# Kernel optimization log

Hardware: AMD Instinct MI355X
Metric: run time of the kernel (lower is better)

Reference implementation:

```python
import jax, jax.numpy as jnp
import numpy as np

B, D_IN, D_OUT, E, TOP_K = 8192, 1024, 512, 8, 2  # D_OUT here is gate hidden = D_IN//2
OUT_DIM = 1024
LN_EPS = 1e-5


def setup_inputs() -> dict:
    key = jax.random.key(0)
    ks = jax.random.split(key, 5)
    s_in = 1.0 / np.sqrt(D_IN)
    s_h = 1.0 / np.sqrt(D_OUT)
    return {
        "x": jax.random.normal(ks[0], (B, D_IN), jnp.float32),
        "gate_w1": jax.random.normal(ks[1], (D_IN, D_OUT), jnp.float32) * s_in,
        "gate_b1": jnp.zeros((D_OUT,), jnp.float32),
        "gate_w2": jax.random.normal(ks[2], (D_OUT, E), jnp.float32) * s_h,
        "gate_b2": jnp.zeros((E,), jnp.float32),
        "We": jax.random.normal(ks[3], (E, D_IN, OUT_DIM), jnp.float32) * s_in,
        "be": jnp.zeros((E, OUT_DIM), jnp.float32),
        "ln_g": jnp.ones((E, OUT_DIM), jnp.float32),
        "ln_b": jnp.zeros((E, OUT_DIM), jnp.float32),
    }


def reference(x, gate_w1, gate_b1, gate_w2, gate_b2, We, be, ln_g, ln_b):
    # Gating network: Linear -> GELU (exact) -> Linear
    g = jax.nn.gelu(x @ gate_w1 + gate_b1, approximate=False)
    scores = g @ gate_w2 + gate_b2                       # [B, E]
    topk_s, topk_i = jax.lax.top_k(scores, TOP_K)        # [B, K]
    topk_w = jax.nn.softmax(topk_s, axis=-1)             # softmax over the top-k only
    # Scatter top-k weights into dense per-expert weights [B, E]
    rows = jnp.arange(scores.shape[0])[:, None]
    dense_w = jnp.zeros_like(scores).at[rows, topk_i].add(topk_w)
    # All-expert forward (non-selected experts get weight 0): Linear -> LayerNorm -> GELU
    h = jnp.einsum("bi,eio->beo", x, We) + be            # [B, E, O]
    mu = h.mean(axis=-1, keepdims=True)
    var = jnp.mean(jnp.square(h - mu), axis=-1, keepdims=True)
    h = (h - mu) * jax.lax.rsqrt(var + LN_EPS) * ln_g + ln_b
    h = jax.nn.gelu(h, approximate=False)
    # Weighted combine (Dropout is identity in eval mode)
    return jnp.einsum("beo,be->bo", h, dense_w)          # [B, O]
```

## Files before the change

### kernel.cpp

```cpp
#include <hip/hip_runtime.h>
#include <hip/hip_bf16.h>
#include <math.h>

#define B_ROWS 8192
#define D_INK  1024
#define D_H    512
#define N_E    8
#define OUT_D  1024
#define LN_EPS 1e-5f
#define GAP_TAU 3e-3f

typedef _Float16 f16x8 __attribute__((ext_vector_type(8)));
typedef _Float16 f16x4v __attribute__((ext_vector_type(4)));
typedef float    f32x4  __attribute__((ext_vector_type(4)));

#define GLOBAL_AS __attribute__((address_space(1)))
#define LDS_AS    __attribute__((address_space(3)))

__device__ __forceinline__ void async16(const void* gptr, void* lptr) {
  __builtin_amdgcn_global_load_lds((const GLOBAL_AS unsigned int*)gptr,
                                   (LDS_AS unsigned int*)lptr, 16, 0, 0);
}

__device__ __forceinline__ float gelu_exact(float x) {
  return 0.5f * x * (1.0f + erff(x * 0.707106781186547524f));
}
__device__ __forceinline__ float clamp_diag(float v) {
  return fminf(fmaxf(v, -1e15f), 1e15f);
}

__global__ __launch_bounds__(256) void convert_x_kernel(
    const float4* __restrict__ x4, f16x4v* __restrict__ hi4) {
  int i = blockIdx.x * 256 + threadIdx.x;
  float4 v = x4[i];
  f16x4v h;
  h[0] = (_Float16)v.x; h[1] = (_Float16)v.y;
  h[2] = (_Float16)v.z; h[3] = (_Float16)v.w;
  hi4[i] = h;
}

__global__ void transpose_split_kernel(const float* __restrict__ src,
                                       _Float16* __restrict__ hi,
                                       int R, int C) {
  __shared__ float tile[32][33];
  long base = (long)blockIdx.z * R * C;
  int c0 = blockIdx.x * 32, r0 = blockIdx.y * 32;
  int tx = threadIdx.x, ty = threadIdx.y;
#pragma unroll
  for (int i = ty; i < 32; i += 8)
    tile[i][tx] = src[base + (long)(r0 + i) * C + (c0 + tx)];
  __syncthreads();
#pragma unroll
  for (int i = ty; i < 32; i += 8)
    hi[base + (long)(c0 + i) * R + (r0 + tx)] = (_Float16)tile[tx][i];
}


__global__ __launch_bounds__(256) void gate_gemm_kernel(
    const _Float16* __restrict__ xh, const _Float16* __restrict__ wh,
    const float* __restrict__ b1, float* __restrict__ g) {
  __shared__ __align__(16) unsigned short Ah[128 * 64];
  __shared__ __align__(16) unsigned short Bh[128 * 64];
  int tid = threadIdx.x, lane = tid & 63, wave = tid >> 6;
  int wm = wave >> 1, wn = wave & 1;
  int n0 = blockIdx.x * 128, m0 = blockIdx.y * 128;

  const char* pah[4]; const char* pbh[4];
#pragma unroll
  for (int i = 0; i < 4; ++i) {
    int f = i * 256 + tid;
    int rowt = f >> 3, slot = f & 7;
    int seg = slot ^ (rowt & 7);
    pah[i] = (const char*)xh + (long)(m0 + rowt) * (D_INK * 2) + seg * 16;
    pbh[i] = (const char*)wh + (long)(n0 + rowt) * (D_INK * 2) + seg * 16;
  }
  f32x4 acc[4][4];
#pragma unroll
  for (int mi = 0; mi < 4; ++mi)
#pragma unroll
    for (int ni = 0; ni < 4; ++ni) acc[mi][ni] = (f32x4){0.f, 0.f, 0.f, 0.f};

  int cl = lane & 15, quad = lane >> 4;
  for (int k0 = 0; k0 < D_INK; k0 += 64) {
#pragma unroll
    for (int i = 0; i < 4; ++i) {
      async16(pah[i] + (long)k0 * 2, (char*)Ah + (i * 256 + wave * 64) * 16);
      async16(pbh[i] + (long)k0 * 2, (char*)Bh + (i * 256 + wave * 64) * 16);
    }
    __syncthreads();
#pragma unroll
    for (int ks = 0; ks < 2; ++ks) {
      f16x8 ah[4], bh[4];
#pragma unroll
      for (int mi = 0; mi < 4; ++mi) {
        int row = wm * 64 + mi * 16 + cl;
        ah[mi] = *(const f16x8*)((const char*)Ah + row * 128 +
                                 (((ks * 4 + quad) ^ (cl & 7)) * 16));
      }
#pragma unroll
      for (int ni = 0; ni < 4; ++ni) {
        int row = wn * 64 + ni * 16 + cl;
        bh[ni] = *(const f16x8*)((const char*)Bh + row * 128 +
                                 (((ks * 4 + quad) ^ (cl & 7)) * 16));
      }
#pragma unroll
      for (int mi = 0; mi < 4; ++mi)
#pragma unroll
        for (int ni = 0; ni < 4; ++ni)
          acc[mi][ni] = __builtin_amdgcn_mfma_f32_16x16x32_f16(ah[mi], bh[ni], acc[mi][ni], 0, 0, 0);
    }
    __syncthreads();
  }
#pragma unroll
  for (int mi = 0; mi < 4; ++mi)
#pragma unroll
    for (int r = 0; r < 4; ++r) {
      int row = m0 + wm * 64 + mi * 16 + quad * 4 + r;
#pragma unroll
      for (int ni = 0; ni < 4; ++ni) {
        int col = n0 + wn * 64 + ni * 16 + cl;
        float v = clamp_diag(acc[mi][ni][r] + b1[col]);
        g[(long)row * D_H + col] = gelu_exact(v);
      }
    }
}

__global__ __launch_bounds__(256) void score_kernel(
    const float* __restrict__ g, const float* __restrict__ w2,
    const float* __restrict__ b2, float* __restrict__ scores,
    int* __restrict__ nflag, int* __restrict__ worklist) {
  int tid = threadIdx.x, lane = tid & 63, wave = tid >> 6;
  int b = blockIdx.x * 4 + wave;
  const float* grow = g + (long)b * D_H + lane * 8;
  float4 g0 = *(const float4*)grow;
  float4 g1 = *(const float4*)(grow + 4);
  float gv[8] = {g0.x, g0.y, g0.z, g0.w, g1.x, g1.y, g1.z, g1.w};
  float acc[8];
#pragma unroll
  for (int e = 0; e < 8; ++e) acc[e] = 0.f;
#pragma unroll
  for (int j = 0; j < 8; ++j) {
    const float* wrow = w2 + (lane * 8 + j) * N_E;
#pragma unroll
    for (int e = 0; e < 8; ++e) acc[e] += gv[j] * wrow[e];
  }
#pragma unroll
  for (int off = 32; off >= 1; off >>= 1)
#pragma unroll
    for (int e = 0; e < 8; ++e) acc[e] += __shfl_xor(acc[e], off, 64);
  if (lane == 0) {
    float s[8];
#pragma unroll
    for (int e = 0; e < 8; ++e) { s[e] = acc[e] + b2[e]; scores[b * N_E + e] = s[e]; }
    int i0 = 0;
#pragma unroll
    for (int e = 1; e < 8; ++e) if (s[e] > s[i0]) i0 = e;
    int i1 = (i0 == 0) ? 1 : 0;
#pragma unroll
    for (int e = 0; e < 8; ++e) if (e != i0 && s[e] > s[i1]) i1 = e;
    float s2 = -3e38f;
#pragma unroll
    for (int e = 0; e < 8; ++e) if (e != i0 && e != i1 && s[e] > s2) s2 = s[e];
    if (s[i1] - s2 < GAP_TAU) {
      int idx = atomicAdd(nflag, 1);
      worklist[idx] = b;
    }
  }
}

__global__ __launch_bounds__(256) void fixup_g_kernel(
    const float* __restrict__ x, const float* __restrict__ w1,
    const float* __restrict__ b1, const int* __restrict__ nflag,
    const int* __restrict__ worklist, double* __restrict__ g64) {
  int n = *nflag;
  int total = n * 2;
  for (int t = blockIdx.x; t < total; t += gridDim.x) {
    int w = t >> 1, half = t & 1;
    int row = worklist[w];
    int col = half * 256 + threadIdx.x;
    const float* xr = x + (long)row * D_INK;
    double a0 = 0.0, a1 = 0.0, a2 = 0.0, a3 = 0.0;
    for (int k = 0; k < D_INK; k += 4) {
      a0 += (double)xr[k + 0] * (double)w1[(long)(k + 0) * D_H + col];
      a1 += (double)xr[k + 1] * (double)w1[(long)(k + 1) * D_H + col];
      a2 += (double)xr[k + 2] * (double)w1[(long)(k + 2) * D_H + col];
      a3 += (double)xr[k + 3] * (double)w1[(long)(k + 3) * D_H + col];
    }
    double s = ((a0 + a1) + (a2 + a3)) + (double)b1[col];
    g64[(long)w * D_H + col] = 0.5 * s * (1.0 + erf(s * 0.70710678118654752440));
  }
}

__global__ __launch_bounds__(256) void fixup_score_kernel(
    const double* __restrict__ g64, const float* __restrict__ w2,
    const float* __restrict__ b2, const int* __restrict__ nflag,
    const int* __restrict__ worklist, float* __restrict__ scores) {
  __shared__ double p2[256];
  int n = *nflag;
  int tid = threadIdx.x;
  for (int w = blockIdx.x; w < n; w += gridDim.x) {
    int row = worklist[w];
    int e = tid & 7, seg = tid >> 3;
    double s = 0.0;
#pragma unroll
    for (int q = seg * 16; q < seg * 16 + 16; ++q)
      s += g64[(long)w * D_H + q] * (double)w2[q * N_E + e];
    p2[tid] = s;
    __syncthreads();
    if (tid < N_E) {
      double t = 0.0;
      for (int i = 0; i < 32; ++i) t += p2[i * 8 + tid];
      scores[row * N_E + tid] = (float)(t + (double)b2[tid]);
    }
    __syncthreads();
  }
}

__global__ __launch_bounds__(256) void select_kernel(
    const float* __restrict__ scores, int* __restrict__ counts,
    int* __restrict__ bucket, float* __restrict__ pair_w,
    int* __restrict__ pair_e) {
  __shared__ int lcnt[N_E];
  __shared__ int lbase[N_E];
  int tid = threadIdx.x;
  int b = blockIdx.x * 256 + tid;
  if (tid < N_E) lcnt[tid] = 0;
  __syncthreads();
  float s[8];
#pragma unroll
  for (int e = 0; e < 8; ++e) s[e] = scores[b * N_E + e];
  int i0 = 0;
#pragma unroll
  for (int e = 1; e < 8; ++e) if (s[e] > s[i0]) i0 = e;
  int i1 = (i0 == 0) ? 1 : 0;
#pragma unroll
  for (int e = 0; e < 8; ++e) if (e != i0 && s[e] > s[i1]) i1 = e;
  float z = expf(s[i1] - s[i0]);
  float inv = 1.0f / (1.0f + z);
  int r0 = atomicAdd(&lcnt[i0], 1);
  int r1 = atomicAdd(&lcnt[i1], 1);
  __syncthreads();
  if (tid < N_E) lbase[tid] = atomicAdd(&counts[tid], lcnt[tid]);
  __syncthreads();
  int p0 = 2 * b, p1 = 2 * b + 1;
  pair_e[p0] = i0; pair_w[p0] = inv;
  pair_e[p1] = i1; pair_w[p1] = z * inv;
  bucket[i0 * B_ROWS + lbase[i0] + r0] = p0;
  bucket[i1 * B_ROWS + lbase[i1] + r1] = p1;
}

__global__ __launch_bounds__(512) void expert_gemm_kernel(
    const _Float16* __restrict__ xh, const _Float16* __restrict__ wet,
    const int* __restrict__ counts, const int* __restrict__ bucket,
    __bf16* __restrict__ h) {
  int nt = blockIdx.x, mt = blockIdx.y, e = blockIdx.z;
  int cnt = counts[e];
  if (mt * 256 >= cnt) return;
  __shared__ __align__(16) unsigned short As[256 * 64];
  __shared__ __align__(16) unsigned short Bs[256 * 64];
  __shared__ int dest_s[256];
  int tid = threadIdx.x, lane = tid & 63, wave = tid >> 6;
  int wm = wave >> 2, wn = wave & 3;
  int n0 = nt * 256;
  if (tid < 256) {
    int idx = mt * 256 + tid;
    dest_s[tid] = (idx < cnt) ? bucket[e * B_ROWS + idx] : 0;
  }
  __syncthreads();
  const char* xb = (const char*)xh;
  const char* wb = (const char*)wet + (long)e * (D_INK * OUT_D * 2);
  const char* aptr[4];
  const char* bptr[4];
#pragma unroll
  for (int i = 0; i < 4; ++i) {
    int f = i * 512 + tid;
    int rowt = f >> 3, slot = f & 7;
    int seg = slot ^ (rowt & 7);
    int rowid = dest_s[rowt] >> 1;
    aptr[i] = xb + (long)rowid * (D_INK * 2) + seg * 16;
    bptr[i] = wb + (long)(n0 + rowt) * (D_INK * 2) + seg * 16;
  }
  f32x4 acc[8][4];
#pragma unroll
  for (int mi = 0; mi < 8; ++mi)
#pragma unroll
    for (int ni = 0; ni < 4; ++ni) acc[mi][ni] = (f32x4){0.f, 0.f, 0.f, 0.f};

  int cl = lane & 15, quad = lane >> 4;
  for (int k0 = 0; k0 < D_INK; k0 += 64) {
#pragma unroll
    for (int i = 0; i < 4; ++i) {
      async16(aptr[i] + (long)k0 * 2, (char*)As + (i * 512 + wave * 64) * 16);
      async16(bptr[i] + (long)k0 * 2, (char*)Bs + (i * 512 + wave * 64) * 16);
    }
    __syncthreads();
#pragma unroll
    for (int ks = 0; ks < 2; ++ks) {
      f16x8 bfr[4];
#pragma unroll
      for (int ni = 0; ni < 4; ++ni) {
        int row = wn * 64 + ni * 16 + cl;
        bfr[ni] = *(const f16x8*)((const char*)Bs + row * 128 +
                                  (((ks * 4 + quad) ^ (cl & 7)) * 16));
      }
#pragma unroll
      for (int mi = 0; mi < 8; ++mi) {
        int row = wm * 128 + mi * 16 + cl;
        f16x8 af = *(const f16x8*)((const char*)As + row * 128 +
                                   (((ks * 4 + quad) ^ (cl & 7)) * 16));
#pragma unroll
        for (int ni = 0; ni < 4; ++ni)
          acc[mi][ni] = __builtin_amdgcn_mfma_f32_16x16x32_f16(af, bfr[ni], acc[mi][ni], 0, 0, 0);
      }
    }
    __syncthreads();
  }
#pragma unroll
  for (int mi = 0; mi < 8; ++mi)
#pragma unroll
    for (int r = 0; r < 4; ++r) {
      int row256 = wm * 128 + mi * 16 + quad * 4 + r;
      if (mt * 256 + row256 < cnt) {
        long dest = dest_s[row256];
        __bf16* hp = h + dest * OUT_D + n0 + wn * 64 + cl;
#pragma unroll
        for (int ni = 0; ni < 4; ++ni)
          hp[ni * 16] = (__bf16)clamp_diag(acc[mi][ni][r]);
      }
    }
}

__global__ __launch_bounds__(256) void ln_combine_kernel(
    const __bf16* __restrict__ h, const float* __restrict__ pair_w,
    const int* __restrict__ pair_e, const float* __restrict__ be,
    const float* __restrict__ ln_g, const float* __restrict__ ln_b,
    float* __restrict__ out) {
  int b = blockIdx.x, tid = threadIdx.x;
  int lane = tid & 63, wave = tid >> 6;
  int c0 = tid * 4;
  __shared__ float red[4][4];
  float hv[2][4];
  float stats[4];
  int ei[2]; float wi[2];
#pragma unroll
  for (int k = 0; k < 2; ++k) {
    int p = 2 * b + k;
    ei[k] = pair_e[p]; wi[k] = pair_w[p];
    const unsigned short* hp = (const unsigned short*)(h + (long)p * OUT_D) + c0;
    ushort4 raw = *(const ushort4*)hp;
    float4 bev = *(const float4*)(be + ei[k] * OUT_D + c0);
    float v0 = __uint_as_float((unsigned)raw.x << 16) + bev.x;
    float v1 = __uint_as_float((unsigned)raw.y << 16) + bev.y;
    float v2 = __uint_as_float((unsigned)raw.z << 16) + bev.z;
    float v3 = __uint_as_float((unsigned)raw.w << 16) + bev.w;
    hv[k][0] = v0; hv[k][1] = v1; hv[k][2] = v2; hv[k][3] = v3;
    stats[2 * k] = v0 + v1 + v2 + v3;
    stats[2 * k + 1] = v0 * v0 + v1 * v1 + v2 * v2 + v3 * v3;
  }
#pragma unroll
  for (int off = 32; off >= 1; off >>= 1)
#pragma unroll
    for (int i = 0; i < 4; ++i) stats[i] += __shfl_xor(stats[i], off, 64);
  if (lane == 0) {
#pragma unroll
    for (int i = 0; i < 4; ++i) red[wave][i] = stats[i];
  }
  __syncthreads();
  float tot[4] = {0.f, 0.f, 0.f, 0.f};
#pragma unroll
  for (int w = 0; w < 4; ++w)
#pragma unroll
    for (int i = 0; i < 4; ++i) tot[i] += red[w][i];
  float outv[4] = {0.f, 0.f, 0.f, 0.f};
#pragma unroll
  for (int k = 0; k < 2; ++k) {
    float mean = tot[2 * k] * (1.0f / OUT_D);
    float var = tot[2 * k + 1] * (1.0f / OUT_D) - mean * mean;
    float rstd = rsqrtf(fmaxf(var, 0.f) + LN_EPS);
    float4 gp = *(const float4*)(ln_g + ei[k] * OUT_D + c0);
    float4 bp = *(const float4*)(ln_b + ei[k] * OUT_D + c0);
    float t0 = (hv[k][0] - mean) * rstd * gp.x + bp.x;
    float t1 = (hv[k][1] - mean) * rstd * gp.y + bp.y;
    float t2 = (hv[k][2] - mean) * rstd * gp.z + bp.z;
    float t3 = (hv[k][3] - mean) * rstd * gp.w + bp.w;
    outv[0] += wi[k] * gelu_exact(t0);
    outv[1] += wi[k] * gelu_exact(t1);
    outv[2] += wi[k] * gelu_exact(t2);
    outv[3] += wi[k] * gelu_exact(t3);
  }
  float4 o; o.x = outv[0]; o.y = outv[1]; o.z = outv[2]; o.w = outv[3];
  *(float4*)(out + (long)b * OUT_D + c0) = o;
}

extern "C" void kernel_launch(void* const* d_in, const int* in_sizes, int n_in,
                              void* d_out, int out_size, void* d_ws, size_t ws_size,
                              hipStream_t stream) {
  const float* x       = (const float*)d_in[0];
  const float* gate_w1 = (const float*)d_in[1];
  const float* gate_b1 = (const float*)d_in[2];
  const float* gate_w2 = (const float*)d_in[3];
  const float* gate_b2 = (const float*)d_in[4];
  const float* We      = (const float*)d_in[5];
  const float* be      = (const float*)d_in[6];
  const float* ln_g    = (const float*)d_in[7];
  const float* ln_b    = (const float*)d_in[8];
  float* out = (float*)d_out;

  char* ws = (char*)d_ws;
  size_t off = 0;
  _Float16* x16h = (_Float16*)(ws + off); off += (size_t)B_ROWS * D_INK * 2;
  _Float16* w1th = (_Float16*)(ws + off); off += (size_t)D_H * D_INK * 2;
  _Float16* wet  = (_Float16*)(ws + off); off += (size_t)N_E * D_INK * OUT_D * 2;
  float* g       = (float*)(ws + off); off += (size_t)B_ROWS * D_H * 4;
  float* scores  = (float*)(ws + off); off += (size_t)B_ROWS * N_E * 4;
  int* counts    = (int*)(ws + off);   off += 64;
  int* nflag     = counts + 8;
  int* worklist  = (int*)(ws + off);   off += (size_t)B_ROWS * 4;
  int* bucket    = (int*)(ws + off);   off += (size_t)N_E * B_ROWS * 4;
  float* pair_w  = (float*)(ws + off); off += (size_t)2 * B_ROWS * 4;
  int* pair_e    = (int*)(ws + off);   off += (size_t)2 * B_ROWS * 4;
  __bf16* h      = (__bf16*)(ws + off); off += (size_t)2 * B_ROWS * OUT_D * 2;
  double* g64    = (double*)h;

  hipMemsetAsync(counts, 0, 64, stream);
  convert_x_kernel<<<B_ROWS * D_INK / 4 / 256, 256, 0, stream>>>(
      (const float4*)x, (f16x4v*)x16h);
  transpose_split_kernel<<<dim3(D_H / 32, D_INK / 32, 1), dim3(32, 8), 0, stream>>>(
      gate_w1, w1th, D_INK, D_H);
  transpose_split_kernel<<<dim3(OUT_D / 32, D_INK / 32, N_E), dim3(32, 8), 0, stream>>>(
      We, wet, D_INK, OUT_D);
  gate_gemm_kernel<<<dim3(D_H / 128, B_ROWS / 128), 256, 0, stream>>>(
      x16h, w1th, gate_b1, g);
  score_kernel<<<B_ROWS / 4, 256, 0, stream>>>(
      g, gate_w2, gate_b2, scores, nflag, worklist);
  fixup_g_kernel<<<512, 256, 0, stream>>>(
      x, gate_w1, gate_b1, nflag, worklist, g64);
  fixup_score_kernel<<<128, 256, 0, stream>>>(
      g64, gate_w2, gate_b2, nflag, worklist, scores);
  select_kernel<<<B_ROWS / 256, 256, 0, stream>>>(
      scores, counts, bucket, pair_w, pair_e);
  expert_gemm_kernel<<<dim3(OUT_D / 256, B_ROWS / 256, N_E), 512, 0, stream>>>(
      x16h, wet, counts, bucket, h);
  ln_combine_kernel<<<B_ROWS, 256, 0, stream>>>(
      h, pair_w, pair_e, be, ln_g, ln_b, out);
}
```

Baseline: 322.8 us.

## Double-buffer LDS in gate and expert GEMMs, shrink expert tiles to 128

Result: no change. 324.8 us (+0.6%).

```diff
diff --git a/kernel.cpp b/kernel.cpp
--- a/kernel.cpp
+++ b/kernel.cpp
@@ -56,11 +56,47 @@
 }
 
 
+__device__ __forceinline__ void stage8(const char* const (&ap)[4],
+                                       const char* const (&bp)[4], long koff,
+                                       char* Ab, char* Bb, int wave) {
+#pragma unroll
+  for (int i = 0; i < 4; ++i) {
+    async16(ap[i] + koff, Ab + (i * 256 + wave * 64) * 16);
+    async16(bp[i] + koff, Bb + (i * 256 + wave * 64) * 16);
+  }
+}
+
+__device__ __forceinline__ void tile_compute(const char* Ab, const char* Bb,
+                                             int wm, int wn, int cl, int quad,
+                                             f32x4 (&acc)[4][4]) {
+#pragma unroll
+  for (int ks = 0; ks < 2; ++ks) {
+    f16x8 ah[4], bh[4];
+#pragma unroll
+    for (int mi = 0; mi < 4; ++mi) {
+      int row = wm * 64 + mi * 16 + cl;
+      ah[mi] = *(const f16x8*)(Ab + row * 128 + (((ks * 4 + quad) ^ (cl & 7)) * 16));
+    }
+#pragma unroll
+    for (int ni = 0; ni < 4; ++ni) {
+      int row = wn * 64 + ni * 16 + cl;
+      bh[ni] = *(const f16x8*)(Bb + row * 128 + (((ks * 4 + quad) ^ (cl & 7)) * 16));
+    }
+#pragma unroll
+    for (int mi = 0; mi < 4; ++mi)
+#pragma unroll
+      for (int ni = 0; ni < 4; ++ni)
+        acc[mi][ni] = __builtin_amdgcn_mfma_f32_16x16x32_f16(ah[mi], bh[ni], acc[mi][ni], 0, 0, 0);
+  }
+}
+
 __global__ __launch_bounds__(256) void gate_gemm_kernel(
     const _Float16* __restrict__ xh, const _Float16* __restrict__ wh,
     const float* __restrict__ b1, float* __restrict__ g) {
-  __shared__ __align__(16) unsigned short Ah[128 * 64];
-  __shared__ __align__(16) unsigned short Bh[128 * 64];
+  __shared__ __align__(16) unsigned short Ah0[128 * 64];
+  __shared__ __align__(16) unsigned short Bh0[128 * 64];
+  __shared__ __align__(16) unsigned short Ah1[128 * 64];
+  __shared__ __align__(16) unsigned short Bh1[128 * 64];
   int tid = threadIdx.x, lane = tid & 63, wave = tid >> 6;
   int wm = wave >> 1, wn = wave & 1;
   int n0 = blockIdx.x * 128, m0 = blockIdx.y * 128;
@@ -81,34 +117,14 @@
     for (int ni = 0; ni < 4; ++ni) acc[mi][ni] = (f32x4){0.f, 0.f, 0.f, 0.f};
 
   int cl = lane & 15, quad = lane >> 4;
-  for (int k0 = 0; k0 < D_INK; k0 += 64) {
-#pragma unroll
-    for (int i = 0; i < 4; ++i) {
-      async16(pah[i] + (long)k0 * 2, (char*)Ah + (i * 256 + wave * 64) * 16);
-      async16(pbh[i] + (long)k0 * 2, (char*)Bh + (i * 256 + wave * 64) * 16);
-    }
-    __syncthreads();
-#pragma unroll
-    for (int ks = 0; ks < 2; ++ks) {
-      f16x8 ah[4], bh[4];
-#pragma unroll
-      for (int mi = 0; mi < 4; ++mi) {
-        int row = wm * 64 + mi * 16 + cl;
-        ah[mi] = *(const f16x8*)((const char*)Ah + row * 128 +
-                                 (((ks * 4 + quad) ^ (cl & 7)) * 16));
-      }
-#pragma unroll
-      for (int ni = 0; ni < 4; ++ni) {
-        int row = wn * 64 + ni * 16 + cl;
-        bh[ni] = *(const f16x8*)((const char*)Bh + row * 128 +
-                                 (((ks * 4 + quad) ^ (cl & 7)) * 16));
-      }
-#pragma unroll
-      for (int mi = 0; mi < 4; ++mi)
-#pragma unroll
-        for (int ni = 0; ni < 4; ++ni)
-          acc[mi][ni] = __builtin_amdgcn_mfma_f32_16x16x32_f16(ah[mi], bh[ni], acc[mi][ni], 0, 0, 0);
-    }
+  stage8(pah, pbh, 0, (char*)Ah0, (char*)Bh0, wave);
+  __syncthreads();
+  for (int s = 0; s < 16; s += 2) {
+    stage8(pah, pbh, (long)(s + 1) * 128, (char*)Ah1, (char*)Bh1, wave);
+    tile_compute((const char*)Ah0, (const char*)Bh0, wm, wn, cl, quad, acc);
+    __syncthreads();
+    if (s + 2 < 16) stage8(pah, pbh, (long)(s + 2) * 128, (char*)Ah0, (char*)Bh0, wave);
+    tile_compute((const char*)Ah1, (const char*)Bh1, wm, wn, cl, quad, acc);
     __syncthreads();
   }
 #pragma unroll
@@ -249,21 +265,25 @@
   bucket[i1 * B_ROWS + lbase[i1] + r1] = p1;
 }
 
-__global__ __launch_bounds__(512) void expert_gemm_kernel(
+__global__ __launch_bounds__(256) void expert_gemm_kernel(
     const _Float16* __restrict__ xh, const _Float16* __restrict__ wet,
     const int* __restrict__ counts, const int* __restrict__ bucket,
     __bf16* __restrict__ h) {
-  int nt = blockIdx.x, mt = blockIdx.y, e = blockIdx.z;
+  int bid = blockIdx.x;
+  int e = bid & 7, seq = bid >> 3;
+  int mt = seq >> 3, nt = seq & 7;
   int cnt = counts[e];
-  if (mt * 256 >= cnt) return;
-  __shared__ __align__(16) unsigned short As[256 * 64];
-  __shared__ __align__(16) unsigned short Bs[256 * 64];
-  __shared__ int dest_s[256];
+  if (mt * 128 >= cnt) return;
+  __shared__ __align__(16) unsigned short As0[128 * 64];
+  __shared__ __align__(16) unsigned short Bs0[128 * 64];
+  __shared__ __align__(16) unsigned short As1[128 * 64];
+  __shared__ __align__(16) unsigned short Bs1[128 * 64];
+  __shared__ int dest_s[128];
   int tid = threadIdx.x, lane = tid & 63, wave = tid >> 6;
-  int wm = wave >> 2, wn = wave & 3;
-  int n0 = nt * 256;
-  if (tid < 256) {
-    int idx = mt * 256 + tid;
+  int wm = wave >> 1, wn = wave & 1;
+  int n0 = nt * 128;
+  if (tid < 128) {
+    int idx = mt * 128 + tid;
     dest_s[tid] = (idx < cnt) ? bucket[e * B_ROWS + idx] : 0;
   }
   __syncthreads();
@@ -273,55 +293,37 @@
   const char* bptr[4];
 #pragma unroll
   for (int i = 0; i < 4; ++i) {
-    int f = i * 512 + tid;
+    int f = i * 256 + tid;
     int rowt = f >> 3, slot = f & 7;
     int seg = slot ^ (rowt & 7);
     int rowid = dest_s[rowt] >> 1;
     aptr[i] = xb + (long)rowid * (D_INK * 2) + seg * 16;
     bptr[i] = wb + (long)(n0 + rowt) * (D_INK * 2) + seg * 16;
   }
-  f32x4 acc[8][4];
-#pragma unroll
-  for (int mi = 0; mi < 8; ++mi)
+  f32x4 acc[4][4];
+#pragma unroll
+  for (int mi = 0; mi < 4; ++mi)
 #pragma unroll
     for (int ni = 0; ni < 4; ++ni) acc[mi][ni] = (f32x4){0.f, 0.f, 0.f, 0.f};
 
   int cl = lane & 15, quad = lane >> 4;
-  for (int k0 = 0; k0 < D_INK; k0 += 64) {
-#pragma unroll
-    for (int i = 0; i < 4; ++i) {
-      async16(aptr[i] + (long)k0 * 2, (char*)As + (i * 512 + wave * 64) * 16);
-      async16(bptr[i] + (long)k0 * 2, (char*)Bs + (i * 512 + wave * 64) * 16);
-    }
-    __syncthreads();
-#pragma unroll
-    for (int ks = 0; ks < 2; ++ks) {
-      f16x8 bfr[4];
-#pragma unroll
-      for (int ni = 0; ni < 4; ++ni) {
-        int row = wn * 64 + ni * 16 + cl;
-        bfr[ni] = *(const f16x8*)((const char*)Bs + row * 128 +
-                                  (((ks * 4 + quad) ^ (cl & 7)) * 16));
-      }
-#pragma unroll
-      for (int mi = 0; mi < 8; ++mi) {
-        int row = wm * 128 + mi * 16 + cl;
-        f16x8 af = *(const f16x8*)((const char*)As + row * 128 +
-                                   (((ks * 4 + quad) ^ (cl & 7)) * 16));
-#pragma unroll
-        for (int ni = 0; ni < 4; ++ni)
-          acc[mi][ni] = __builtin_amdgcn_mfma_f32_16x16x32_f16(af, bfr[ni], acc[mi][ni], 0, 0, 0);
-      }
-    }
-    __syncthreads();
-  }
-#pragma unroll
-  for (int mi = 0; mi < 8; ++mi)
+  stage8(aptr, bptr, 0, (char*)As0, (char*)Bs0, wave);
+  __syncthreads();
+  for (int s = 0; s < 16; s += 2) {
+    stage8(aptr, bptr, (long)(s + 1) * 128, (char*)As1, (char*)Bs1, wave);
+    tile_compute((const char*)As0, (const char*)Bs0, wm, wn, cl, quad, acc);
+    __syncthreads();
+    if (s + 2 < 16) stage8(aptr, bptr, (long)(s + 2) * 128, (char*)As0, (char*)Bs0, wave);
+    tile_compute((const char*)As1, (const char*)Bs1, wm, wn, cl, quad, acc);
+    __syncthreads();
+  }
+#pragma unroll
+  for (int mi = 0; mi < 4; ++mi)
 #pragma unroll
     for (int r = 0; r < 4; ++r) {
-      int row256 = wm * 128 + mi * 16 + quad * 4 + r;
-      if (mt * 256 + row256 < cnt) {
-        long dest = dest_s[row256];
+      int row128 = wm * 64 + mi * 16 + quad * 4 + r;
+      if (mt * 128 + row128 < cnt) {
+        long dest = dest_s[row128];
         __bf16* hp = h + dest * OUT_D + n0 + wn * 64 + cl;
 #pragma unroll
         for (int ni = 0; ni < 4; ++ni)
@@ -439,7 +441,7 @@
       g64, gate_w2, gate_b2, nflag, worklist, scores);
   select_kernel<<<B_ROWS / 256, 256, 0, stream>>>(
       scores, counts, bucket, pair_w, pair_e);
-  expert_gemm_kernel<<<dim3(OUT_D / 256, B_ROWS / 256, N_E), 512, 0, stream>>>(
+  expert_gemm_kernel<<<N_E * (B_ROWS / 128) * (OUT_D / 128), 256, 0, stream>>>(
       x16h, wet, counts, bucket, h);
   ln_combine_kernel<<<B_ROWS, 256, 0, stream>>>(
       h, pair_w, pair_e, be, ln_g, ln_b, out);
```

## Double-buffer expert GEMM LDS tiles and interleave prefetch with MFMA phases

Applied to the files above, without the earlier changes.

Result: slower. 334.2 us (+3.5%).

```diff
diff --git a/kernel.cpp b/kernel.cpp
--- a/kernel.cpp
+++ b/kernel.cpp
@@ -56,6 +56,40 @@
 }
 
 
+__device__ __forceinline__ void stage8(const char* const (&ap)[4],
+                                       const char* const (&bp)[4], long koff,
+                                       char* Ab, char* Bb, int wave) {
+#pragma unroll
+  for (int i = 0; i < 4; ++i) {
+    async16(ap[i] + koff, Ab + (i * 256 + wave * 64) * 16);
+    async16(bp[i] + koff, Bb + (i * 256 + wave * 64) * 16);
+  }
+}
+
+__device__ __forceinline__ void tile_compute(const char* Ab, const char* Bb,
+                                             int wm, int wn, int cl, int quad,
+                                             f32x4 (&acc)[4][4]) {
+#pragma unroll
+  for (int ks = 0; ks < 2; ++ks) {
+    f16x8 ah[4], bh[4];
+#pragma unroll
+    for (int mi = 0; mi < 4; ++mi) {
+      int row = wm * 64 + mi * 16 + cl;
+      ah[mi] = *(const f16x8*)(Ab + row * 128 + (((ks * 4 + quad) ^ (cl & 7)) * 16));
+    }
+#pragma unroll
+    for (int ni = 0; ni < 4; ++ni) {
+      int row = wn * 64 + ni * 16 + cl;
+      bh[ni] = *(const f16x8*)(Bb + row * 128 + (((ks * 4 + quad) ^ (cl & 7)) * 16));
+    }
+#pragma unroll
+    for (int mi = 0; mi < 4; ++mi)
+#pragma unroll
+      for (int ni = 0; ni < 4; ++ni)
+        acc[mi][ni] = __builtin_amdgcn_mfma_f32_16x16x32_f16(ah[mi], bh[ni], acc[mi][ni], 0, 0, 0);
+  }
+}
+
 __global__ __launch_bounds__(256) void gate_gemm_kernel(
     const _Float16* __restrict__ xh, const _Float16* __restrict__ wh,
     const float* __restrict__ b1, float* __restrict__ g) {
@@ -82,33 +116,9 @@
 
   int cl = lane & 15, quad = lane >> 4;
   for (int k0 = 0; k0 < D_INK; k0 += 64) {
-#pragma unroll
-    for (int i = 0; i < 4; ++i) {
-      async16(pah[i] + (long)k0 * 2, (char*)Ah + (i * 256 + wave * 64) * 16);
-      async16(pbh[i] + (long)k0 * 2, (char*)Bh + (i * 256 + wave * 64) * 16);
-    }
+    stage8(pah, pbh, (long)k0 * 2, (char*)Ah, (char*)Bh, wave);
     __syncthreads();
-#pragma unroll
-    for (int ks = 0; ks < 2; ++ks) {
-      f16x8 ah[4], bh[4];
-#pragma unroll
-      for (int mi = 0; mi < 4; ++mi) {
-        int row = wm * 64 + mi * 16 + cl;
-        ah[mi] = *(const f16x8*)((const char*)Ah + row * 128 +
-                                 (((ks * 4 + quad) ^ (cl & 7)) * 16));
-      }
-#pragma unroll
-      for (int ni = 0; ni < 4; ++ni) {
-        int row = wn * 64 + ni * 16 + cl;
-        bh[ni] = *(const f16x8*)((const char*)Bh + row * 128 +
-                                 (((ks * 4 + quad) ^ (cl & 7)) * 16));
-      }
-#pragma unroll
-      for (int mi = 0; mi < 4; ++mi)
-#pragma unroll
-        for (int ni = 0; ni < 4; ++ni)
-          acc[mi][ni] = __builtin_amdgcn_mfma_f32_16x16x32_f16(ah[mi], bh[ni], acc[mi][ni], 0, 0, 0);
-    }
+    tile_compute((const char*)Ah, (const char*)Bh, wm, wn, cl, quad, acc);
     __syncthreads();
   }
 #pragma unroll
@@ -256,8 +266,8 @@
   int nt = blockIdx.x, mt = blockIdx.y, e = blockIdx.z;
   int cnt = counts[e];
   if (mt * 256 >= cnt) return;
-  __shared__ __align__(16) unsigned short As[256 * 64];
-  __shared__ __align__(16) unsigned short Bs[256 * 64];
+  __shared__ __align__(16) unsigned short As[2][256 * 64];
+  __shared__ __align__(16) unsigned short Bs[2][256 * 64];
   __shared__ int dest_s[256];
   int tid = threadIdx.x, lane = tid & 63, wave = tid >> 6;
   int wm = wave >> 2, wn = wave & 3;
@@ -267,17 +277,14 @@
     dest_s[tid] = (idx < cnt) ? bucket[e * B_ROWS + idx] : 0;
   }
   __syncthreads();
-  const char* xb = (const char*)xh;
   const char* wb = (const char*)wet + (long)e * (D_INK * OUT_D * 2);
-  const char* aptr[4];
-  const char* bptr[4];
+  const char* aptr[4]; const char* bptr[4];
 #pragma unroll
   for (int i = 0; i < 4; ++i) {
     int f = i * 512 + tid;
     int rowt = f >> 3, slot = f & 7;
     int seg = slot ^ (rowt & 7);
-    int rowid = dest_s[rowt] >> 1;
-    aptr[i] = xb + (long)rowid * (D_INK * 2) + seg * 16;
+    aptr[i] = (const char*)xh + (long)(dest_s[rowt] >> 1) * (D_INK * 2) + seg * 16;
     bptr[i] = wb + (long)(n0 + rowt) * (D_INK * 2) + seg * 16;
   }
   f32x4 acc[8][4];
@@ -287,33 +294,58 @@
     for (int ni = 0; ni < 4; ++ni) acc[mi][ni] = (f32x4){0.f, 0.f, 0.f, 0.f};
 
   int cl = lane & 15, quad = lane >> 4;
-  for (int k0 = 0; k0 < D_INK; k0 += 64) {
-#pragma unroll
-    for (int i = 0; i < 4; ++i) {
-      async16(aptr[i] + (long)k0 * 2, (char*)As + (i * 512 + wave * 64) * 16);
-      async16(bptr[i] + (long)k0 * 2, (char*)Bs + (i * 512 + wave * 64) * 16);
-    }
-    __syncthreads();
-#pragma unroll
-    for (int ks = 0; ks < 2; ++ks) {
-      f16x8 bfr[4];
+#pragma unroll
+  for (int i = 0; i < 4; ++i) {
+    async16(aptr[i], (char*)As[0] + (i * 512 + wave * 64) * 16);
+    async16(bptr[i], (char*)Bs[0] + (i * 512 + wave * 64) * 16);
+  }
+  asm volatile("s_waitcnt vmcnt(0)" ::: "memory");
+  __builtin_amdgcn_s_barrier();
+
+  for (int t = 0; t < 16; ++t) {
+    int cur = t & 1;
+    const char* Ab = (const char*)As[cur];
+    const char* Bb = (const char*)Bs[cur];
+    char* An = (char*)As[cur ^ 1];
+    char* Bn = (char*)Bs[cur ^ 1];
+    long koff = (long)(t + 1) * 128;
+#pragma unroll
+    for (int q = 0; q < 4; ++q) {
+      if (t < 15) {
+        if (q == 0) {
+#pragma unroll
+          for (int i = 0; i < 4; ++i)
+            async16(aptr[i] + koff, An + (i * 512 + wave * 64) * 16);
+        } else if (q == 1) {
+#pragma unroll
+          for (int i = 0; i < 4; ++i)
+            async16(bptr[i] + koff, Bn + (i * 512 + wave * 64) * 16);
+        }
+      }
+      int ks = q >> 1, mh = (q & 1) * 4;
+      f16x8 af[4], bfr[4];
 #pragma unroll
       for (int ni = 0; ni < 4; ++ni) {
         int row = wn * 64 + ni * 16 + cl;
-        bfr[ni] = *(const f16x8*)((const char*)Bs + row * 128 +
-                                  (((ks * 4 + quad) ^ (cl & 7)) * 16));
+        bfr[ni] = *(const f16x8*)(Bb + row * 128 + (((ks * 4 + quad) ^ (cl & 7)) * 16));
       }
 #pragma unroll
-      for (int mi = 0; mi < 8; ++mi) {
-        int row = wm * 128 + mi * 16 + cl;
-        f16x8 af = *(const f16x8*)((const char*)As + row * 128 +
-                                   (((ks * 4 + quad) ^ (cl & 7)) * 16));
+      for (int mi = 0; mi < 4; ++mi) {
+        int row = wm * 128 + (mh + mi) * 16 + cl;
+        af[mi] = *(const f16x8*)(Ab + row * 128 + (((ks * 4 + quad) ^ (cl & 7)) * 16));
+      }
+      __builtin_amdgcn_s_setprio(1);
+#pragma unroll
+      for (int mi = 0; mi < 4; ++mi)
 #pragma unroll
         for (int ni = 0; ni < 4; ++ni)
-          acc[mi][ni] = __builtin_amdgcn_mfma_f32_16x16x32_f16(af, bfr[ni], acc[mi][ni], 0, 0, 0);
-      }
-    }
-    __syncthreads();
+          acc[mh + mi][ni] = __builtin_amdgcn_mfma_f32_16x16x32_f16(
+              af[mi], bfr[ni], acc[mh + mi][ni], 0, 0, 0);
+      __builtin_amdgcn_s_setprio(0);
+      if (q == 3 && t < 15)
+        asm volatile("s_waitcnt vmcnt(0)" ::: "memory");
+      __builtin_amdgcn_s_barrier();
+    }
   }
 #pragma unroll
   for (int mi = 0; mi < 8; ++mi)
```
